# Kernel tuning notes

Hardware: AMD Instinct MI355X
Metric: run time of the kernel (lower is better)

Reference implementation:

```python
import jax, jax.numpy as jnp
import numpy as np

C, H, P = 128, 4, 8  # d_model, n_heads, n_points (n_levels=1)
D = C // H


def setup_inputs() -> dict:
    key = jax.random.key(0)
    ks = jax.random.split(key, 14)
    B, Y, X = 2, 200, 200
    N = Y * X
    s = 0.05
    inp = {
        "query": jax.random.normal(ks[0], (B, N, C), jnp.float32),
        "query_pos": jax.random.normal(ks[1], (B, N, C), jnp.float32),
        # MSDeformAttn params
        "Wv": jax.random.normal(ks[2], (C, C), jnp.float32) * s,
        "bv": jnp.zeros((C,), jnp.float32),
        "Woff": jax.random.normal(ks[3], (C, H * P * 2), jnp.float32) * s,
        "boff": jax.random.normal(ks[4], (H * P * 2,), jnp.float32) * s,
        "Wattn": jax.random.normal(ks[5], (C, H * P), jnp.float32) * s,
        "battn": jnp.zeros((H * P,), jnp.float32),
        "Wout1": jax.random.normal(ks[6], (C, C), jnp.float32) * s,  # MSDeformAttn.output_proj
        "bout1": jnp.zeros((C,), jnp.float32),
        "Wout2": jax.random.normal(ks[7], (C, C), jnp.float32) * s,  # wrapper output_proj
        "bout2": jnp.zeros((C,), jnp.float32),
        "Y": Y,
        "X": X,
    }
    return inp


def _deform_attn(q, v_in, Wv, bv, Woff, boff, Wattn, battn, Wout1, bout1, Y, X):
    B, N, _ = q.shape
    # reference points: grid centers, stacked (y, x) normalized (as in source)
    ref_y = (jnp.arange(Y, dtype=jnp.float32) + 0.5) / Y
    ref_x = (jnp.arange(X, dtype=jnp.float32) + 0.5) / X
    ry, rx = jnp.meshgrid(ref_y, ref_x, indexing="ij")
    ref = jnp.stack([ry.reshape(-1), rx.reshape(-1)], -1)  # (N, 2)

    value = (v_in @ Wv + bv).reshape(B, Y, X, H, D).transpose(0, 3, 1, 2, 4)  # (B,H,Y,X,D)
    off = (q @ Woff + boff).reshape(B, N, H, P, 2)
    attn = jax.nn.softmax((q @ Wattn + battn).reshape(B, N, H, P), axis=-1)

    # offset normalizer = (W, H) = (X, Y); loc = ref + off/norm  (faithful to source)
    norm = jnp.array([X, Y], jnp.float32)
    loc = ref[None, :, None, None, :] + off / norm  # (B,N,H,P,2)

    # grid_sample bilinear, align_corners=False, zero padding; channel 0 = x, 1 = y
    gx = loc[..., 0] * X - 0.5
    gy = loc[..., 1] * Y - 0.5
    x0 = jnp.floor(gx)
    y0 = jnp.floor(gy)
    wx1 = gx - x0
    wy1 = gy - y0
    x0i = x0.astype(jnp.int32)
    y0i = y0.astype(jnp.int32)

    b_idx = jnp.arange(B)[:, None, None, None]
    h_idx = jnp.arange(H)[None, None, :, None]

    def gather(yi, xi, w):
        valid = (yi >= 0) & (yi < Y) & (xi >= 0) & (xi < X)
        yc = jnp.clip(yi, 0, Y - 1)
        xc = jnp.clip(xi, 0, X - 1)
        v = value[b_idx, h_idx, yc, xc]  # (B,N,H,P,D)
        return v * (w * valid)[..., None]

    sampled = (
        gather(y0i, x0i, (1 - wy1) * (1 - wx1))
        + gather(y0i, x0i + 1, (1 - wy1) * wx1)
        + gather(y0i + 1, x0i, wy1 * (1 - wx1))
        + gather(y0i + 1, x0i + 1, wy1 * wx1)
    )
    out = (sampled * attn[..., None]).sum(axis=3).reshape(B, N, C)
    return out @ Wout1 + bout1


def reference(query, query_pos, Wv, bv, Woff, boff, Wattn, battn, Wout1, bout1, Wout2, bout2, Y, X):
    residual = query
    q = query + query_pos
    out = _deform_attn(q, q, Wv, bv, Woff, boff, Wattn, battn, Wout1, bout1, Y, X)
    out = out @ Wout2 + bout2  # wrapper output_proj; dropout in eval mode = identity
    return out + residual
```

## Files before the change

### kernel.cpp

```cpp
#include <hip/hip_runtime.h>
#include <hip/hip_bf16.h>

#define BQ 2
#define YY 200
#define XX 200
#define NQ 40000
#define CC 128
#define MTOT 80000
#define NCOL 224
#define NTILES 5000

typedef __attribute__((ext_vector_type(8))) short short8;
typedef __attribute__((ext_vector_type(4))) short short4v;
typedef __attribute__((ext_vector_type(4))) float f32x4;
typedef __attribute__((ext_vector_type(2))) float f32x2;

static __device__ __forceinline__ unsigned short f2bf(float f) {
    union { float f; unsigned int u; } v; v.f = f;
    unsigned int r = v.u + 0x7FFF + ((v.u >> 16) & 1);
    return (unsigned short)(r >> 16);
}
static __device__ __forceinline__ unsigned short f2bf_hw(float f) {
    __hip_bfloat16 h = __float2bfloat16(f);
    unsigned short s;
    __builtin_memcpy(&s, &h, 2);
    return s;
}

__global__ void prep_wcat(const float* __restrict__ Wv, const float* __restrict__ Woff,
                          const float* __restrict__ Wattn, unsigned short* __restrict__ WcatT) {
    int idx = blockIdx.x * 256 + threadIdx.x;
    if (idx >= NCOL * CC) return;
    int c = idx >> 7, k = idx & 127;
    float w = (c < 128) ? Wv[k * 128 + c]
            : (c < 192) ? Woff[k * 64 + (c - 128)]
                        : Wattn[k * 32 + (c - 192)];
    WcatT[c * 128 + k] = f2bf(w);
}

__global__ void prep_w12(const float* __restrict__ Wout1, const float* __restrict__ Wout2,
                         const float* __restrict__ bout1, const float* __restrict__ bout2,
                         unsigned short* __restrict__ W12T, float* __restrict__ b12) {
    int idx = blockIdx.x * 256 + threadIdx.x;
    int c = idx >> 7, k = idx & 127;
    float s = 0.f;
    for (int j = 0; j < 128; ++j) s += Wout1[k * 128 + j] * Wout2[j * 128 + c];
    W12T[c * 128 + k] = f2bf(s);
    if (k == 0) {
        float t = bout2[c];
        for (int j = 0; j < 128; ++j) t += bout1[j] * Wout2[j * 128 + c];
        b12[c] = t;
    }
}

__global__ __launch_bounds__(256) void qsum_kernel(const float* __restrict__ query,
                                                   const float* __restrict__ qpos,
                                                   unsigned short* __restrict__ qbf) {
    const size_t total = (size_t)MTOT * CC / 8;
    for (size_t c = (size_t)blockIdx.x * 256 + threadIdx.x; c < total;
         c += (size_t)gridDim.x * 256) {
        const float4* a = (const float4*)(query + c * 8);
        const float4* b = (const float4*)(qpos + c * 8);
        float4 a0 = a[0], a1 = a[1], b0 = b[0], b1 = b[1];
        short8 w;
        w[0] = (short)f2bf_hw(a0.x + b0.x); w[1] = (short)f2bf_hw(a0.y + b0.y);
        w[2] = (short)f2bf_hw(a0.z + b0.z); w[3] = (short)f2bf_hw(a0.w + b0.w);
        w[4] = (short)f2bf_hw(a1.x + b1.x); w[5] = (short)f2bf_hw(a1.y + b1.y);
        w[6] = (short)f2bf_hw(a1.z + b1.z); w[7] = (short)f2bf_hw(a1.w + b1.w);
        *(short8*)(qbf + c * 8) = w;
    }
}

__global__ __launch_bounds__(256, 2) void g1_kernel(
    const unsigned short* __restrict__ qbf, const unsigned short* __restrict__ WcatT,
    const float* __restrict__ bv, const float* __restrict__ boff, const float* __restrict__ battn,
    unsigned short* __restrict__ value_bf, float* __restrict__ off_out, float* __restrict__ logits_out)
{
    const int tid = threadIdx.x;
    const int group = blockIdx.x >> 8;
    const int gblk = blockIdx.x & 255;
    const int lane = tid & 63;
    const int arow = lane & 15, kq = lane >> 4;
    const int wid = gblk * 4 + (tid >> 6);
    const int tg0 = group * 4;
    const int NT = (group == 3) ? 2 : 4;

    short8 bf[4][4];
#pragma unroll
    for (int t = 0; t < 4; ++t) {
        if (t < NT) {
#pragma unroll
            for (int ks = 0; ks < 4; ++ks)
                bf[t][ks] = *(const short8*)(WcatT + (size_t)((tg0 + t) * 16 + arow) * 128 + ks * 32 + kq * 8);
        }
    }

    f32x4 biasv[4];
#pragma unroll
    for (int t = 0; t < 4; ++t) {
        if (t < NT) {
            const float* bp = (group < 2) ? (bv + (tg0 + t) * 16 + kq * 4)
                            : (group == 2) ? (boff + (tg0 + t - 8) * 16 + kq * 4)
                                           : (battn + (tg0 + t - 12) * 16 + kq * 4);
            float4 b4 = *(const float4*)bp;
            biasv[t] = (f32x4){b4.x, b4.y, b4.z, b4.w};
        }
    }

    for (int tile = wid; tile < NTILES; tile += 1024) {
        const char* pa = (const char*)qbf + (size_t)(tile * 16 + arow) * 256 + kq * 16;
        short8 af[4];
#pragma unroll
        for (int ks = 0; ks < 4; ++ks) af[ks] = *(const short8*)(pa + ks * 64);

        f32x4 acc[4];
#pragma unroll
        for (int t = 0; t < 4; ++t) acc[t] = biasv[t];

#pragma unroll
        for (int ks = 0; ks < 4; ++ks) {
#pragma unroll
            for (int t = 0; t < 4; ++t) {
                if (t < NT)
                    acc[t] = __builtin_amdgcn_mfma_f32_16x16x32_bf16(bf[t][ks], af[ks], acc[t], 0, 0, 0);
            }
        }

        const int row = tile * 16 + arow;
        if (group < 2) {
#pragma unroll
            for (int t = 0; t < 4; ++t) {
                short4v pv;
                pv[0] = (short)f2bf_hw(acc[t][0]); pv[1] = (short)f2bf_hw(acc[t][1]);
                pv[2] = (short)f2bf_hw(acc[t][2]); pv[3] = (short)f2bf_hw(acc[t][3]);
                *(short4v*)(value_bf + (size_t)row * 128 + (tg0 + t) * 16 + kq * 4) = pv;
            }
        } else if (group == 2) {
#pragma unroll
            for (int t = 0; t < 4; ++t) {
                float4 o = make_float4(acc[t][0], acc[t][1], acc[t][2], acc[t][3]);
                *(float4*)(off_out + (size_t)row * 64 + (tg0 + t - 8) * 16 + kq * 4) = o;
            }
        } else {
#pragma unroll
            for (int t = 0; t < 2; ++t) {
                float4 o = make_float4(acc[t][0], acc[t][1], acc[t][2], acc[t][3]);
                *(float4*)(logits_out + (size_t)row * 32 + (tg0 + t - 12) * 16 + kq * 4) = o;
            }
        }
    }
}

__global__ __launch_bounds__(256) void sample_kernel(
    const unsigned short* __restrict__ value_bf, const float* __restrict__ off_in,
    const float* __restrict__ logits, unsigned short* __restrict__ sampled)
{
    __shared__ int4 SA[8][33];
    __shared__ int4 SW[8][33];

    const int tid = threadIdx.x;
    const int qi = tid >> 5;
    const int lane = tid & 31;
    const int r = blockIdx.x * 8 + qi;
    const int b = (r >= NQ) ? 1 : 0;
    const int n = r - b * NQ;
    const int yq = n / XX, xq = n - yq * XX;

    {
        float lg = logits[(size_t)r * 32 + lane];
        float m = lg;
        m = fmaxf(m, __shfl_xor(m, 1));
        m = fmaxf(m, __shfl_xor(m, 2));
        m = fmaxf(m, __shfl_xor(m, 4));
        float e = __expf(lg - m);
        float s = e;
        s += __shfl_xor(s, 1);
        s += __shfl_xor(s, 2);
        s += __shfl_xor(s, 4);
        float aw = e / s;

        float2 o = ((const float2*)(off_in + (size_t)r * 64))[lane];
        float gx = (float)yq + o.x;
        float gy = (float)xq + o.y;
        float fx = floorf(gx), fy = floorf(gy);
        int x0 = (int)fx, y0 = (int)fy;
        float wx1 = gx - fx, wy1 = gy - fy;
        float vx0 = ((unsigned)x0 < XX) ? 1.f : 0.f;
        float vx1 = ((unsigned)(x0 + 1) < XX) ? 1.f : 0.f;
        float vy0 = ((unsigned)y0 < YY) ? 1.f : 0.f;
        float vy1 = ((unsigned)(y0 + 1) < YY) ? 1.f : 0.f;
        int x0c = min(max(x0, 0), XX - 1);
        int x1c = min(max(x0 + 1, 0), XX - 1);
        int y0c = min(max(y0, 0), YY - 1);
        int y1c = min(max(y0 + 1, 0), YY - 1);
        int hb = (lane >> 3) * 64;
        int rowA = y0c * XX, rowB = y1c * XX;
        int4 addrs;
        addrs.x = (rowA + x0c) * 256 + hb;
        addrs.y = (rowA + x1c) * 256 + hb;
        addrs.z = (rowB + x0c) * 256 + hb;
        addrs.w = (rowB + x1c) * 256 + hb;
        int4 wts;
        wts.x = __float_as_int((1.f - wx1) * vx0);
        wts.y = __float_as_int(wx1 * vx1);
        wts.z = __float_as_int(aw * (1.f - wy1) * vy0);
        wts.w = __float_as_int(aw * wy1 * vy1);
        const int slot = (lane & 15) * 2 + (lane >> 4);
        SA[qi][slot] = addrs;
        SW[qi][slot] = wts;
    }
    __syncthreads();

    const char* vb = (const char*)(value_bf + (size_t)b * NQ * 128);
    const int cb = (lane & 15) * 4;
    const int g16 = lane >> 4;

    f32x2 acc[2][2];
    acc[0][0] = (f32x2){0.f, 0.f}; acc[0][1] = (f32x2){0.f, 0.f};
    acc[1][0] = (f32x2){0.f, 0.f}; acc[1][1] = (f32x2){0.f, 0.f};

#pragma unroll
    for (int i = 0; i < 16; ++i) {
        const int slot = 2 * i + g16;
        int4 ai = SA[qi][slot];
        int4 wi = SW[qi][slot];
        f32x2 wxa2 = (f32x2){__int_as_float(wi.x), __int_as_float(wi.x)};
        f32x2 wxb2 = (f32x2){__int_as_float(wi.y), __int_as_float(wi.y)};
        f32x2 wya2 = (f32x2){__int_as_float(wi.z), __int_as_float(wi.z)};
        f32x2 wyb2 = (f32x2){__int_as_float(wi.w), __int_as_float(wi.w)};

        unsigned int u00 = *(const unsigned int*)(vb + ai.x + cb);
        unsigned int u01 = *(const unsigned int*)(vb + ai.y + cb);
        unsigned int u10 = *(const unsigned int*)(vb + ai.z + cb);
        unsigned int u11 = *(const unsigned int*)(vb + ai.w + cb);

        f32x2 f00 = (f32x2){__uint_as_float(u00 << 16), __uint_as_float(u00 & 0xFFFF0000u)};
        f32x2 f01 = (f32x2){__uint_as_float(u01 << 16), __uint_as_float(u01 & 0xFFFF0000u)};
        f32x2 f10 = (f32x2){__uint_as_float(u10 << 16), __uint_as_float(u10 & 0xFFFF0000u)};
        f32x2 f11 = (f32x2){__uint_as_float(u11 << 16), __uint_as_float(u11 & 0xFFFF0000u)};

        f32x2 ta = __builtin_elementwise_fma(wxa2, f00, wxb2 * f01);
        f32x2 tb = __builtin_elementwise_fma(wxa2, f10, wxb2 * f11);

        const int j = i >> 3, k = i & 1;
        acc[j][k] = __builtin_elementwise_fma(wya2, ta, acc[j][k]);
        acc[j][k] = __builtin_elementwise_fma(wyb2, tb, acc[j][k]);
    }

    char* sp = (char*)(sampled + (size_t)r * 128);
#pragma unroll
    for (int j = 0; j < 2; ++j) {
        f32x2 a2 = acc[j][0] + acc[j][1];
        unsigned int packed = ((unsigned int)f2bf(a2[1]) << 16) | (unsigned int)f2bf(a2[0]);
        *(unsigned int*)(sp + (g16 * 2 + j) * 64 + cb) = packed;
    }
}

__global__ __launch_bounds__(256, 2) void g2_kernel(
    const unsigned short* __restrict__ sampled, const unsigned short* __restrict__ W12T,
    const float* __restrict__ b12, const float* __restrict__ query, float* __restrict__ out)
{
    const int tid = threadIdx.x;
    const int group = blockIdx.x >> 9;
    const int gblk = blockIdx.x & 511;
    const int lane = tid & 63;
    const int arow = lane & 15, kq = lane >> 4;
    const int wid = gblk * 4 + (tid >> 6);
    const int tg0 = group * 4;

    short8 bf[4][4];
#pragma unroll
    for (int t = 0; t < 4; ++t)
#pragma unroll
        for (int ks = 0; ks < 4; ++ks)
            bf[t][ks] = *(const short8*)(W12T + (size_t)((tg0 + t) * 16 + arow) * 128 + ks * 32 + kq * 8);

    f32x4 biasv[4];
#pragma unroll
    for (int t = 0; t < 4; ++t) {
        float4 b4 = *(const float4*)(b12 + (tg0 + t) * 16 + kq * 4);
        biasv[t] = (f32x4){b4.x, b4.y, b4.z, b4.w};
    }

    for (int tile = wid; tile < NTILES; tile += 2048) {
        const char* pa = (const char*)sampled + (size_t)(tile * 16 + arow) * 256 + kq * 16;
        short8 af[4];
#pragma unroll
        for (int ks = 0; ks < 4; ++ks) af[ks] = *(const short8*)(pa + ks * 64);

        f32x4 acc[4];
#pragma unroll
        for (int t = 0; t < 4; ++t) acc[t] = biasv[t];

#pragma unroll
        for (int ks = 0; ks < 4; ++ks)
#pragma unroll
            for (int t = 0; t < 4; ++t)
                acc[t] = __builtin_amdgcn_mfma_f32_16x16x32_bf16(bf[t][ks], af[ks], acc[t], 0, 0, 0);

        const int row = tile * 16 + arow;
#pragma unroll
        for (int t = 0; t < 4; ++t) {
            size_t idx = (size_t)row * 128 + (tg0 + t) * 16 + kq * 4;
            float4 q4 = *(const float4*)(query + idx);
            float4 o = make_float4(acc[t][0] + q4.x, acc[t][1] + q4.y,
                                   acc[t][2] + q4.z, acc[t][3] + q4.w);
            *(float4*)(out + idx) = o;
        }
    }
}

extern "C" void kernel_launch(void* const* d_in, const int* in_sizes, int n_in,
                              void* d_out, int out_size, void* d_ws, size_t ws_size,
                              hipStream_t stream) {
    const float* query = (const float*)d_in[0];
    const float* qpos  = (const float*)d_in[1];
    const float* Wv    = (const float*)d_in[2];
    const float* bv    = (const float*)d_in[3];
    const float* Woff  = (const float*)d_in[4];
    const float* boff  = (const float*)d_in[5];
    const float* Wattn = (const float*)d_in[6];
    const float* battn = (const float*)d_in[7];
    const float* Wout1 = (const float*)d_in[8];
    const float* bout1 = (const float*)d_in[9];
    const float* Wout2 = (const float*)d_in[10];
    const float* bout2 = (const float*)d_in[11];
    float* out = (float*)d_out;

    char* ws = (char*)d_ws;
    unsigned short* value_bf = (unsigned short*)(ws);
    float*          off_buf  = (float*)(ws + 20480000);
    float*          logits   = (float*)(ws + 40960000);
    unsigned short* sampled  = (unsigned short*)(ws + 51200000);
    unsigned short* WcatT    = (unsigned short*)(ws + 71680000);
    unsigned short* W12T     = (unsigned short*)(ws + 71680000 + 57344);
    float*          b12      = (float*)(ws + 71680000 + 57344 + 32768);

    unsigned short* qbf = sampled;

    prep_wcat<<<112, 256, 0, stream>>>(Wv, Woff, Wattn, WcatT);
    prep_w12<<<64, 256, 0, stream>>>(Wout1, Wout2, bout1, bout2, W12T, b12);
    qsum_kernel<<<2048, 256, 0, stream>>>(query, qpos, qbf);
    g1_kernel<<<1024, 256, 0, stream>>>(qbf, WcatT, bv, boff, battn,
                                        value_bf, off_buf, logits);
    sample_kernel<<<MTOT / 8, 256, 0, stream>>>(value_bf, off_buf, logits, sampled);
    g2_kernel<<<1024, 256, 0, stream>>>(sampled, W12T, b12, query, out);
}
```

Before: 121.0 us.

## Store value tensor in fp16 and bilinear-sample with packed half2 FMAs

```diff
diff --git a/kernel.cpp b/kernel.cpp
--- a/kernel.cpp
+++ b/kernel.cpp
@@ -1,5 +1,6 @@
 #include <hip/hip_runtime.h>
 #include <hip/hip_bf16.h>
+#include <hip/hip_fp16.h>
 
 #define BQ 2
 #define YY 200
@@ -13,7 +14,6 @@
 typedef __attribute__((ext_vector_type(8))) short short8;
 typedef __attribute__((ext_vector_type(4))) short short4v;
 typedef __attribute__((ext_vector_type(4))) float f32x4;
-typedef __attribute__((ext_vector_type(2))) float f32x2;
 
 static __device__ __forceinline__ unsigned short f2bf(float f) {
     union { float f; unsigned int u; } v; v.f = f;
@@ -25,6 +25,15 @@
     unsigned short s;
     __builtin_memcpy(&s, &h, 2);
     return s;
+}
+static __device__ __forceinline__ __half2 u2h2(unsigned int u) {
+    __half2 h; __builtin_memcpy(&h, &u, 4); return h;
+}
+static __device__ __forceinline__ unsigned int h22u(__half2 h) {
+    unsigned int u; __builtin_memcpy(&u, &h, 4); return u;
+}
+static __device__ __forceinline__ short h2s(__half h) {
+    short s; __builtin_memcpy(&s, &h, 2); return s;
 }
 
 __global__ void prep_wcat(const float* __restrict__ Wv, const float* __restrict__ Woff,
@@ -74,7 +83,7 @@
 __global__ __launch_bounds__(256, 2) void g1_kernel(
     const unsigned short* __restrict__ qbf, const unsigned short* __restrict__ WcatT,
     const float* __restrict__ bv, const float* __restrict__ boff, const float* __restrict__ battn,
-    unsigned short* __restrict__ value_bf, float* __restrict__ off_out, float* __restrict__ logits_out)
+    unsigned short* __restrict__ value_h, float* __restrict__ off_out, float* __restrict__ logits_out)
 {
     const int tid = threadIdx.x;
     const int group = blockIdx.x >> 8;
@@ -131,9 +140,9 @@
 #pragma unroll
             for (int t = 0; t < 4; ++t) {
                 short4v pv;
-                pv[0] = (short)f2bf_hw(acc[t][0]); pv[1] = (short)f2bf_hw(acc[t][1]);
-                pv[2] = (short)f2bf_hw(acc[t][2]); pv[3] = (short)f2bf_hw(acc[t][3]);
-                *(short4v*)(value_bf + (size_t)row * 128 + (tg0 + t) * 16 + kq * 4) = pv;
+                pv[0] = h2s(__float2half(acc[t][0])); pv[1] = h2s(__float2half(acc[t][1]));
+                pv[2] = h2s(__float2half(acc[t][2])); pv[3] = h2s(__float2half(acc[t][3]));
+                *(short4v*)(value_h + (size_t)row * 128 + (tg0 + t) * 16 + kq * 4) = pv;
             }
         } else if (group == 2) {
 #pragma unroll
@@ -152,7 +161,7 @@
 }
 
 __global__ __launch_bounds__(256) void sample_kernel(
-    const unsigned short* __restrict__ value_bf, const float* __restrict__ off_in,
+    const unsigned short* __restrict__ value_h, const float* __restrict__ off_in,
     const float* __restrict__ logits, unsigned short* __restrict__ sampled)
 {
     __shared__ int4 SA[8][33];
@@ -200,60 +209,64 @@
         addrs.y = (rowA + x1c) * 256 + hb;
         addrs.z = (rowB + x0c) * 256 + hb;
         addrs.w = (rowB + x1c) * 256 + hb;
+
+        float wxa = (1.f - wx1) * vx0;
+        float wxb = wx1 * vx1;
+        float wya = aw * (1.f - wy1) * vy0;
+        float wyb = aw * wy1 * vy1;
         int4 wts;
-        wts.x = __float_as_int((1.f - wx1) * vx0);
-        wts.y = __float_as_int(wx1 * vx1);
-        wts.z = __float_as_int(aw * (1.f - wy1) * vy0);
-        wts.w = __float_as_int(aw * wy1 * vy1);
-        const int slot = (lane & 15) * 2 + (lane >> 4);
+        wts.x = (int)h22u(__float2half2_rn(wxa * wya));
+        wts.y = (int)h22u(__float2half2_rn(wxb * wya));
+        wts.z = (int)h22u(__float2half2_rn(wxa * wyb));
+        wts.w = (int)h22u(__float2half2_rn(wxb * wyb));
+
+        const int slot = (lane & 7) * 4 + (lane >> 3);
         SA[qi][slot] = addrs;
         SW[qi][slot] = wts;
     }
     __syncthreads();
 
-    const char* vb = (const char*)(value_bf + (size_t)b * NQ * 128);
-    const int cb = (lane & 15) * 4;
-    const int g16 = lane >> 4;
-
-    f32x2 acc[2][2];
-    acc[0][0] = (f32x2){0.f, 0.f}; acc[0][1] = (f32x2){0.f, 0.f};
-    acc[1][0] = (f32x2){0.f, 0.f}; acc[1][1] = (f32x2){0.f, 0.f};
-
-#pragma unroll
-    for (int i = 0; i < 16; ++i) {
-        const int slot = 2 * i + g16;
+    const char* vb = (const char*)(value_h + (size_t)b * NQ * 128);
+    const int h = lane >> 3, oc = lane & 7;
+    const int cb = oc * 8;
+
+    __half2 accA0 = __float2half2_rn(0.f), accA1 = __float2half2_rn(0.f);
+    __half2 accB0 = __float2half2_rn(0.f), accB1 = __float2half2_rn(0.f);
+
+#pragma unroll
+    for (int p = 0; p < 8; ++p) {
+        const int slot = p * 4 + h;
         int4 ai = SA[qi][slot];
         int4 wi = SW[qi][slot];
-        f32x2 wxa2 = (f32x2){__int_as_float(wi.x), __int_as_float(wi.x)};
-        f32x2 wxb2 = (f32x2){__int_as_float(wi.y), __int_as_float(wi.y)};
-        f32x2 wya2 = (f32x2){__int_as_float(wi.z), __int_as_float(wi.z)};
-        f32x2 wyb2 = (f32x2){__int_as_float(wi.w), __int_as_float(wi.w)};
-
-        unsigned int u00 = *(const unsigned int*)(vb + ai.x + cb);
-        unsigned int u01 = *(const unsigned int*)(vb + ai.y + cb);
-        unsigned int u10 = *(const unsigned int*)(vb + ai.z + cb);
-        unsigned int u11 = *(const unsigned int*)(vb + ai.w + cb);
-
-        f32x2 f00 = (f32x2){__uint_as_float(u00 << 16), __uint_as_float(u00 & 0xFFFF0000u)};
-        f32x2 f01 = (f32x2){__uint_as_float(u01 << 16), __uint_as_float(u01 & 0xFFFF0000u)};
-        f32x2 f10 = (f32x2){__uint_as_float(u10 << 16), __uint_as_float(u10 & 0xFFFF0000u)};
-        f32x2 f11 = (f32x2){__uint_as_float(u11 << 16), __uint_as_float(u11 & 0xFFFF0000u)};
-
-        f32x2 ta = __builtin_elementwise_fma(wxa2, f00, wxb2 * f01);
-        f32x2 tb = __builtin_elementwise_fma(wxa2, f10, wxb2 * f11);
-
-        const int j = i >> 3, k = i & 1;
-        acc[j][k] = __builtin_elementwise_fma(wya2, ta, acc[j][k]);
-        acc[j][k] = __builtin_elementwise_fma(wyb2, tb, acc[j][k]);
-    }
-
-    char* sp = (char*)(sampled + (size_t)r * 128);
-#pragma unroll
-    for (int j = 0; j < 2; ++j) {
-        f32x2 a2 = acc[j][0] + acc[j][1];
-        unsigned int packed = ((unsigned int)f2bf(a2[1]) << 16) | (unsigned int)f2bf(a2[0]);
-        *(unsigned int*)(sp + (g16 * 2 + j) * 64 + cb) = packed;
-    }
+
+        uint2 u00 = *(const uint2*)(vb + ai.x + cb);
+        uint2 u01 = *(const uint2*)(vb + ai.y + cb);
+        uint2 u10 = *(const uint2*)(vb + ai.z + cb);
+        uint2 u11 = *(const uint2*)(vb + ai.w + cb);
+
+        __half2 w00 = u2h2((unsigned int)wi.x);
+        __half2 w01 = u2h2((unsigned int)wi.y);
+        __half2 w10 = u2h2((unsigned int)wi.z);
+        __half2 w11 = u2h2((unsigned int)wi.w);
+
+        accA0 = __hfma2(w00, u2h2(u00.x), accA0);
+        accA1 = __hfma2(w00, u2h2(u00.y), accA1);
+        accA0 = __hfma2(w01, u2h2(u01.x), accA0);
+        accA1 = __hfma2(w01, u2h2(u01.y), accA1);
+        accB0 = __hfma2(w10, u2h2(u10.x), accB0);
+        accB1 = __hfma2(w10, u2h2(u10.y), accB1);
+        accB0 = __hfma2(w11, u2h2(u11.x), accB0);
+        accB1 = __hfma2(w11, u2h2(u11.y), accB1);
+    }
+
+    float c0 = __low2float(accA0) + __low2float(accB0);
+    float c1 = __high2float(accA0) + __high2float(accB0);
+    float c2 = __low2float(accA1) + __low2float(accB1);
+    float c3 = __high2float(accA1) + __high2float(accB1);
+    uint2 packed;
+    packed.x = ((unsigned int)f2bf(c1) << 16) | (unsigned int)f2bf(c0);
+    packed.y = ((unsigned int)f2bf(c3) << 16) | (unsigned int)f2bf(c2);
+    *(uint2*)((char*)(sampled + (size_t)r * 128) + h * 64 + cb) = packed;
 }
 
 __global__ __launch_bounds__(256, 2) void g2_kernel(
@@ -328,7 +341,7 @@
     float* out = (float*)d_out;
 
     char* ws = (char*)d_ws;
-    unsigned short* value_bf = (unsigned short*)(ws);
+    unsigned short* value_h  = (unsigned short*)(ws);
     float*          off_buf  = (float*)(ws + 20480000);
     float*          logits   = (float*)(ws + 40960000);
     unsigned short* sampled  = (unsigned short*)(ws + 51200000);
@@ -342,7 +355,7 @@
     prep_w12<<<64, 256, 0, stream>>>(Wout1, Wout2, bout1, bout2, W12T, b12);
     qsum_kernel<<<2048, 256, 0, stream>>>(query, qpos, qbf);
     g1_kernel<<<1024, 256, 0, stream>>>(qbf, WcatT, bv, boff, battn,
-                                        value_bf, off_buf, logits);
-    sample_kernel<<<MTOT / 8, 256, 0, stream>>>(value_bf, off_buf, logits, sampled);
+                                        value_h, off_buf, logits);
+    sample_kernel<<<MTOT / 8, 256, 0, stream>>>(value_h, off_buf, logits, sampled);
     g2_kernel<<<1024, 256, 0, stream>>>(sampled, W12T, b12, query, out);
 }
```

Result: slower. 124.2 us (+2.7%).
